# Optimization experiments

Hardware: AMD Instinct MI355X
Metric: run time of the kernel (lower is better)

Reference implementation:

```python
import jax, jax.numpy as jnp
import numpy as np

B, CN, CC, D, V = 65536, 16, 16, 128, 65
EPS = 1e-05

def setup_inputs() -> dict:
    key = jax.random.key(0)
    ks = jax.random.split(key, 7)
    x_num = jax.random.normal(ks[0], (B, CN), dtype=jnp.float32)
    x_cat = jax.random.randint(ks[1], (B, CC), 0, V, dtype=jnp.int32)
    means = jax.random.normal(ks[2], (CN,), dtype=jnp.float32)
    stds = jax.random.uniform(ks[3], (CN,), dtype=jnp.float32, minval=0.5, maxval=2.0)
    lin_W = jax.random.normal(ks[4], (CN, D), dtype=jnp.float32) * 0.02  # Linear(1,D) weight per numeric attr
    lin_b = jax.random.normal(ks[5], (CN, D), dtype=jnp.float32) * 0.02
    emb = jax.random.normal(ks[6], (CC, V, D), dtype=jnp.float32) * 0.02  # stacked embedding tables
    return {"x_num": x_num, "means": means, "stds": stds, "lin_W": lin_W,
            "lin_b": lin_b, "emb": emb, "x_cat": x_cat}

def reference(x_num, means, stds, lin_W, lin_b, emb, x_cat):
    # numeric attrs: sigmoid((x - mean)/(std + eps)) -> Linear(1,D), summed over attrs
    z = jax.nn.sigmoid((x_num - means) / (stds + EPS))          # [B, CN]
    h = jnp.einsum('bi,id->bd', z, lin_W) + lin_b.sum(axis=0)   # [B, D]
    # categorical attrs: per-attr embedding lookup, summed over attrs
    gathered = emb[jnp.arange(emb.shape[0]), x_cat]             # [B, CC, D]
    return h + gathered.sum(axis=1)                              # [B, D]
```

## Files before the change

### kernel.cpp

```cpp
#include <hip/hip_runtime.h>


constexpr int CN = 16;
constexpr int CC = 16;
constexpr int D  = 128;
constexpr int V  = 65;
constexpr float EPS = 1e-5f;
constexpr int ROWS_PER_BLOCK = 8;

__global__ __launch_bounds__(256) void embed_att_kernel(
    const float* __restrict__ x_num,
    const float* __restrict__ means,
    const float* __restrict__ stds,
    const float* __restrict__ lin_W,
    const float* __restrict__ lin_b,
    const float* __restrict__ emb,
    const int*  __restrict__ x_cat,
    float* __restrict__ out)
{
    __shared__ float z_s[ROWS_PER_BLOCK][CN];
    __shared__ int   idx_s[ROWS_PER_BLOCK][CC];
    __shared__ float w_s[CN * D];
    __shared__ float bsum_s[D];

    const int tid  = threadIdx.x;
    const int row0 = blockIdx.x * ROWS_PER_BLOCK;

    {
        const float4* w4 = (const float4*)lin_W;
        ((float4*)w_s)[tid]       = w4[tid];
        ((float4*)w_s)[tid + 256] = w4[tid + 256];
    }

    if (tid < D) {
        float s = 0.f;
#pragma unroll
        for (int i = 0; i < CN; ++i) s += lin_b[i * D + tid];
        bsum_s[tid] = s;
    }

    if (tid < ROWS_PER_BLOCK * CN) {
        const int r = tid >> 4, a = tid & 15;
        const float x = x_num[row0 * CN + tid];
        const float m = means[a];
        const float s = stds[a];
        const float t = (x - m) / (s + EPS);
        const float e = __builtin_amdgcn_exp2f(t * -1.44269504088896340736f);
        z_s[r][a]   = 1.0f / (1.0f + e);
        idx_s[r][a] = x_cat[row0 * CC + tid];
    }
    __syncthreads();

    const int r   = tid >> 5;
    const int g   = tid & 31;
    const int row = row0 + r;

    float acc[4];
    {
        const float4 b = ((const float4*)bsum_s)[g];
        acc[0] = b.x; acc[1] = b.y; acc[2] = b.z; acc[3] = b.w;
    }

#pragma unroll
    for (int i = 0; i < CN; ++i) {
        const float zi = z_s[r][i];
        const float4 w = ((const float4*)w_s)[i * 32 + g];
        acc[0] += zi * w.x; acc[1] += zi * w.y;
        acc[2] += zi * w.z; acc[3] += zi * w.w;
    }

#pragma unroll
    for (int c = 0; c < CC; ++c) {
        const int idx = idx_s[r][c];
        const float4 e = *(const float4*)&emb[(c * V + idx) * D + g * 4];
        acc[0] += e.x; acc[1] += e.y; acc[2] += e.z; acc[3] += e.w;
    }

    float4 o; o.x = acc[0]; o.y = acc[1]; o.z = acc[2]; o.w = acc[3];
    *(float4*)&out[row * D + g * 4] = o;
}

extern "C" void kernel_launch(void* const* d_in, const int* in_sizes, int n_in,
                              void* d_out, int out_size, void* d_ws, size_t ws_size,
                              hipStream_t stream) {
    const float* x_num = (const float*)d_in[0];
    const float* means = (const float*)d_in[1];
    const float* stds  = (const float*)d_in[2];
    const float* lin_W = (const float*)d_in[3];
    const float* lin_b = (const float*)d_in[4];
    const float* emb   = (const float*)d_in[5];
    const int*   x_cat = (const int*)d_in[6];
    float* out = (float*)d_out;

    const int nrows = in_sizes[0] / CN;
    const int grid  = nrows / ROWS_PER_BLOCK;

    embed_att_kernel<<<grid, 256, 0, stream>>>(x_num, means, stds, lin_W, lin_b,
                                               emb, x_cat, out);
}
```

Baseline: 99.02 us.

## Slice output columns per block, cache bf16 embedding slice in LDS, double-buffer tiles

```diff
diff --git a/kernel.cpp b/kernel.cpp
--- a/kernel.cpp
+++ b/kernel.cpp
@@ -6,9 +6,33 @@
 constexpr int D  = 128;
 constexpr int V  = 65;
 constexpr float EPS = 1e-5f;
-constexpr int ROWS_PER_BLOCK = 8;
 
-__global__ __launch_bounds__(256) void embed_att_kernel(
+constexpr int W      = 16;
+constexpr int NSLICE = D / W;
+constexpr int RPB    = 512;
+constexpr int TILE   = 64;
+constexpr int NTILE  = RPB / TILE;
+constexpr int PAD    = 20;
+
+__device__ __forceinline__ unsigned short f2bf(float f) {
+    unsigned u = __float_as_uint(f);
+    u = (u + 0x7fffu + ((u >> 16) & 1u)) >> 16;
+    return (unsigned short)u;
+}
+
+__device__ __forceinline__ void fma4(float s, const float4& w, float4& a) {
+    a.x += s * w.x; a.y += s * w.y; a.z += s * w.z; a.w += s * w.w;
+}
+
+__device__ __forceinline__ void gacc(const unsigned short* p, float4& a) {
+    const uint2 g = *(const uint2*)p;
+    a.x += __uint_as_float(g.x << 16);
+    a.y += __uint_as_float(g.x & 0xffff0000u);
+    a.z += __uint_as_float(g.y << 16);
+    a.w += __uint_as_float(g.y & 0xffff0000u);
+}
+
+__global__ __launch_bounds__(256, 3) void embed_att_kernel(
     const float* __restrict__ x_num,
     const float* __restrict__ means,
     const float* __restrict__ stds,
@@ -18,66 +42,94 @@
     const int*  __restrict__ x_cat,
     float* __restrict__ out)
 {
-    __shared__ float z_s[ROWS_PER_BLOCK][CN];
-    __shared__ int   idx_s[ROWS_PER_BLOCK][CC];
-    __shared__ float w_s[CN * D];
-    __shared__ float bsum_s[D];
+    __shared__ unsigned short emb_s[CC * V * W];
+    __shared__ float z_s[2][TILE][PAD];
+    __shared__ int   idx_s[2][TILE][PAD];
 
-    const int tid  = threadIdx.x;
-    const int row0 = blockIdx.x * ROWS_PER_BLOCK;
+    const int tid = threadIdx.x;
+    const int l   = tid & 3;
+    const int l4  = l * 4;
+    const int rr  = tid >> 2;
+    const int d0  = blockIdx.y * W;
+    const int row_base = blockIdx.x * RPB;
 
-    {
-        const float4* w4 = (const float4*)lin_W;
-        ((float4*)w_s)[tid]       = w4[tid];
-        ((float4*)w_s)[tid + 256] = w4[tid + 256];
+    float4 wf[CN];
+    float4 bs = make_float4(0.f, 0.f, 0.f, 0.f);
+#pragma unroll
+    for (int i = 0; i < CN; ++i) {
+        wf[i] = *(const float4*)&lin_W[i * D + d0 + l4];
+        const float4 b = *(const float4*)&lin_b[i * D + d0 + l4];
+        bs.x += b.x; bs.y += b.y; bs.z += b.z; bs.w += b.w;
+    }
+    const float4 mm = *(const float4*)&means[l4];
+    const float4 sv = *(const float4*)&stds[l4];
+    const float LOG2E = 1.44269504088896340736f;
+    float4 inv;
+    inv.x = -LOG2E / (sv.x + EPS); inv.y = -LOG2E / (sv.y + EPS);
+    inv.z = -LOG2E / (sv.z + EPS); inv.w = -LOG2E / (sv.w + EPS);
+
+    for (int j = tid; j < CC * V * W / 4; j += 256) {
+        const int seg = j >> 2, k = j & 3;
+        const float4 e = *(const float4*)&emb[seg * D + d0 + k * 4];
+        uint2 p;
+        p.x = (unsigned)f2bf(e.x) | ((unsigned)f2bf(e.y) << 16);
+        p.y = (unsigned)f2bf(e.z) | ((unsigned)f2bf(e.w) << 16);
+        *(uint2*)&emb_s[seg * W + k * 4] = p;
     }
 
-    if (tid < D) {
-        float s = 0.f;
-#pragma unroll
-        for (int i = 0; i < CN; ++i) s += lin_b[i * D + tid];
-        bsum_s[tid] = s;
+    float4 xf; int4 xi;
+    {
+        const int row = row_base + rr;
+        xf = *(const float4*)&x_num[row * CN + l4];
+        xi = *(const int4*)&x_cat[row * CC + l4];
     }
 
-    if (tid < ROWS_PER_BLOCK * CN) {
-        const int r = tid >> 4, a = tid & 15;
-        const float x = x_num[row0 * CN + tid];
-        const float m = means[a];
-        const float s = stds[a];
-        const float t = (x - m) / (s + EPS);
-        const float e = __builtin_amdgcn_exp2f(t * -1.44269504088896340736f);
-        z_s[r][a]   = 1.0f / (1.0f + e);
-        idx_s[r][a] = x_cat[row0 * CC + tid];
+    for (int t = 0; t < NTILE; ++t) {
+        const int buf = t & 1;
+        float4 z;
+        z.x = 1.f / (1.f + __builtin_amdgcn_exp2f((xf.x - mm.x) * inv.x));
+        z.y = 1.f / (1.f + __builtin_amdgcn_exp2f((xf.y - mm.y) * inv.y));
+        z.z = 1.f / (1.f + __builtin_amdgcn_exp2f((xf.z - mm.z) * inv.z));
+        z.w = 1.f / (1.f + __builtin_amdgcn_exp2f((xf.w - mm.w) * inv.w));
+        *(float4*)&z_s[buf][rr][l4] = z;
+        *(int4*)&idx_s[buf][rr][l4] = xi;
+        __syncthreads();
+
+        if (t + 1 < NTILE) {
+            const int row = row_base + (t + 1) * TILE + rr;
+            xf = *(const float4*)&x_num[row * CN + l4];
+            xi = *(const int4*)&x_cat[row * CC + l4];
+        }
+
+        const int4 i0 = *(const int4*)&idx_s[buf][rr][0];
+        const int4 i1 = *(const int4*)&idx_s[buf][rr][4];
+        const int4 i2 = *(const int4*)&idx_s[buf][rr][8];
+        const int4 i3 = *(const int4*)&idx_s[buf][rr][12];
+        const float4 z0 = *(const float4*)&z_s[buf][rr][0];
+        const float4 z1 = *(const float4*)&z_s[buf][rr][4];
+        const float4 z2 = *(const float4*)&z_s[buf][rr][8];
+        const float4 z3 = *(const float4*)&z_s[buf][rr][12];
+
+        float4 acc = bs;
+        fma4(z0.x, wf[0],  acc); fma4(z0.y, wf[1],  acc);
+        fma4(z0.z, wf[2],  acc); fma4(z0.w, wf[3],  acc);
+        fma4(z1.x, wf[4],  acc); fma4(z1.y, wf[5],  acc);
+        fma4(z1.z, wf[6],  acc); fma4(z1.w, wf[7],  acc);
+        fma4(z2.x, wf[8],  acc); fma4(z2.y, wf[9],  acc);
+        fma4(z2.z, wf[10], acc); fma4(z2.w, wf[11], acc);
+        fma4(z3.x, wf[12], acc); fma4(z3.y, wf[13], acc);
+        fma4(z3.z, wf[14], acc); fma4(z3.w, wf[15], acc);
+
+#define GAT(c, ix) gacc(&emb_s[((c) * V + (ix)) * W + l4], acc)
+        GAT(0,  i0.x); GAT(1,  i0.y); GAT(2,  i0.z); GAT(3,  i0.w);
+        GAT(4,  i1.x); GAT(5,  i1.y); GAT(6,  i1.z); GAT(7,  i1.w);
+        GAT(8,  i2.x); GAT(9,  i2.y); GAT(10, i2.z); GAT(11, i2.w);
+        GAT(12, i3.x); GAT(13, i3.y); GAT(14, i3.z); GAT(15, i3.w);
+#undef GAT
+
+        const int row = row_base + t * TILE + rr;
+        *(float4*)&out[row * D + d0 + l4] = acc;
     }
-    __syncthreads();
-
-    const int r   = tid >> 5;
-    const int g   = tid & 31;
-    const int row = row0 + r;
-
-    float acc[4];
-    {
-        const float4 b = ((const float4*)bsum_s)[g];
-        acc[0] = b.x; acc[1] = b.y; acc[2] = b.z; acc[3] = b.w;
-    }
-
-#pragma unroll
-    for (int i = 0; i < CN; ++i) {
-        const float zi = z_s[r][i];
-        const float4 w = ((const float4*)w_s)[i * 32 + g];
-        acc[0] += zi * w.x; acc[1] += zi * w.y;
-        acc[2] += zi * w.z; acc[3] += zi * w.w;
-    }
-
-#pragma unroll
-    for (int c = 0; c < CC; ++c) {
-        const int idx = idx_s[r][c];
-        const float4 e = *(const float4*)&emb[(c * V + idx) * D + g * 4];
-        acc[0] += e.x; acc[1] += e.y; acc[2] += e.z; acc[3] += e.w;
-    }
-
-    float4 o; o.x = acc[0]; o.y = acc[1]; o.z = acc[2]; o.w = acc[3];
-    *(float4*)&out[row * D + g * 4] = o;
 }
 
 extern "C" void kernel_launch(void* const* d_in, const int* in_sizes, int n_in,
@@ -92,9 +144,10 @@
     const int*   x_cat = (const int*)d_in[6];
     float* out = (float*)d_out;
 
-    const int nrows = in_sizes[0] / CN;
-    const int grid  = nrows / ROWS_PER_BLOCK;
+    const int B      = in_sizes[0] / CN;
+    const int nchunk = B / RPB;
 
+    dim3 grid(nchunk, NSLICE, 1);
     embed_att_kernel<<<grid, 256, 0, stream>>>(x_num, means, stds, lin_W, lin_b,
                                                emb, x_cat, out);
 }
```

New measurement: 99.45 us. About the same (+0.4%).
